# Kernel optimization log

Measured on AMD Instinct MI355X. Metric: run time of the kernel, lower is better.

## Reference

```python
import jax, jax.numpy as jnp
import numpy as np

B, C, H, W = 8, 256, 64, 64
DQK = 16  # int(sqrt(out_channels))


def setup_inputs() -> dict:
    key = jax.random.key(0)
    ks = jax.random.split(key, 8)
    s_in = 1.0 / np.sqrt(C)
    return {
        "x": jax.random.normal(ks[0], (B, C, H, W), dtype=jnp.float32),
        "Wf": jax.random.normal(ks[1], (DQK, C), dtype=jnp.float32) * s_in,
        "bf": jnp.zeros((DQK,), dtype=jnp.float32),
        "Wg": jax.random.normal(ks[2], (DQK, C), dtype=jnp.float32) * s_in,
        "bg": jnp.zeros((DQK,), dtype=jnp.float32),
        "Wh": jax.random.normal(ks[3], (C, C), dtype=jnp.float32) * s_in,
        "bh": jnp.zeros((C,), dtype=jnp.float32),
        # original inits attention_multiplier to 0.0; use small nonzero so output depends on attention path
        "gamma": jnp.float32(0.5),
    }


def reference(x, Wf, bf, Wg, bg, Wh, bh, gamma):
    b, c, h, w = x.shape
    hw = h * w
    # 1x1 convs == per-pixel channel projections
    f = (jnp.einsum('bchw,oc->bohw', x, Wf) + bf[None, :, None, None]).reshape(b, -1, hw)  # [B,DQK,HW]
    g = (jnp.einsum('bchw,oc->bohw', x, Wg) + bg[None, :, None, None]).reshape(b, -1, hw)  # [B,DQK,HW]
    hh = (jnp.einsum('bchw,oc->bohw', x, Wh) + bh[None, :, None, None]).reshape(b, -1, hw)  # [B,C,HW]
    # s[b,n,m] = sum_k g[b,k,n] * f[b,k,m]  -> [B,HW,HW]
    s = jnp.einsum('bkn,bkm->bnm', g, f)
    beta = jax.nn.softmax(s, axis=-1)
    # o = beta @ h^T, then transpose back to channel-first: [B,C,HW]
    o = jnp.einsum('bnm,bcm->bcn', beta, hh)
    return gamma * o.reshape(x.shape) + x
```

## Files before the change

### kernel.cpp

```cpp
#include <hip/hip_runtime.h>
#include <math.h>

#define BATCH 8
#define CH    256
#define HWN   4096
#define DQK   16

typedef __attribute__((ext_vector_type(8))) short short8;
typedef __attribute__((ext_vector_type(4))) float float4v;

__device__ __forceinline__ unsigned short f2bf(float f) {
    union { float f; unsigned int u; } v; v.f = f;
    unsigned int r = v.u + 0x7FFF + ((v.u >> 16) & 1);
    return (unsigned short)(r >> 16);
}
__device__ __forceinline__ unsigned int pack2bf(float lo, float hi) {
    union { float f; unsigned int u; } a, b; a.f = lo; b.f = hi;
    unsigned int ra = (a.u + 0x7FFF + ((a.u >> 16) & 1)) >> 16;
    unsigned int rb = (b.u + 0x7FFF + ((b.u >> 16) & 1)) & 0xFFFF0000u;
    return ra | rb;
}
__device__ __forceinline__ int perm_ft(int m) {
    return (m & ~28) | ((m & 24) >> 1) | ((m & 4) << 2);
}

__global__ __launch_bounds__(256) void wcast_kernel(
    const float* __restrict__ Wf, const float* __restrict__ bf_,
    const float* __restrict__ Wg, const float* __restrict__ bg,
    const float* __restrict__ Wh, const float* __restrict__ bh,
    unsigned short* __restrict__ Wbf, float* __restrict__ bcat)
{
    const int r = blockIdx.x;
    const int t = threadIdx.x;
    const float* src = (r < 16) ? (Wf + r*CH) : (r < 32) ? (Wg + (r-16)*CH) : (Wh + (r-32)*CH);
    Wbf[r*CH + t] = f2bf(src[t]);
    if (t == 0) bcat[r] = (r < 16) ? bf_[r] : (r < 32) ? bg[r-16] : bh[r-32];
}

__global__ __launch_bounds__(256) void xt_kernel(const float* __restrict__ x,
                                                 unsigned short* __restrict__ xt)
{
    const int t  = threadIdx.x;
    const int p0 = blockIdx.x * 64;
    const int c0 = blockIdx.y * 64;
    const int b  = blockIdx.z;
    __shared__ unsigned short tile[64][73];
    const int pc = t & 63;
    const int r0 = (t >> 6) * 16;
    #pragma unroll
    for (int j = 0; j < 16; j++) {
        int c = r0 + j;
        tile[pc][c] = f2bf(x[(size_t)(b*CH + c0 + c)*HWN + p0 + pc]);
    }
    __syncthreads();
    const int pr = t >> 2;
    const int cb = (t & 3) * 16;
    unsigned int outv[8];
    #pragma unroll
    for (int i = 0; i < 8; i++)
        outv[i] = (unsigned int)tile[pr][cb + 2*i] | ((unsigned int)tile[pr][cb + 2*i + 1] << 16);
    unsigned short* dst = &xt[(size_t)(b*HWN + p0 + pr)*CH + c0 + cb];
    *(uint4*)dst       = *(uint4*)&outv[0];
    *(uint4*)(dst + 8) = *(uint4*)&outv[4];
}

__global__ __launch_bounds__(256, 6) void proj_kernel(
    const unsigned short* __restrict__ xt, const unsigned short* __restrict__ Wbf,
    const float* __restrict__ bcat,
    unsigned short* __restrict__ ft, unsigned short* __restrict__ g,
    unsigned short* __restrict__ h3)
{
    const int t      = threadIdx.x;
    const int px0    = blockIdx.x * 64;
    const int b      = blockIdx.y;
    const int rtbase = blockIdx.z * 6;
    const int lane = t & 63, w = t >> 6, l15 = lane & 15, quad = lane >> 4;

    float4v acc[6];
    #pragma unroll
    for (int rt = 0; rt < 6; rt++) acc[rt] = (float4v){0.f,0.f,0.f,0.f};

    const unsigned short* xrow = &xt[((size_t)(b*HWN + px0 + w*16 + l15))*CH + quad*8];
    const unsigned short* wrow = &Wbf[(size_t)l15*CH + quad*8];

    #pragma unroll
    for (int ks = 0; ks < 8; ks++) {
        short8 afrag = *(const short8*)&xrow[ks*32];
        #pragma unroll
        for (int rt = 0; rt < 6; rt++) {
            short8 bfrag = *(const short8*)&wrow[(size_t)(rtbase + rt)*16*CH + ks*32];
            acc[rt] = __builtin_amdgcn_mfma_f32_16x16x32_bf16(afrag, bfrag, acc[rt], 0, 0, 0);
        }
    }

    const int pxl = px0 + w*16 + quad*4;
    const int mt  = (px0 >> 5) + (w >> 1);
    const int sub = ((w & 1)*2 + (quad >> 1))*128 + l15*8 + (quad & 1)*4;
    #pragma unroll
    for (int rt = 0; rt < 6; rt++) {
        const int R = rtbase + rt;
        if (R == 0) {
            float bv = bcat[l15];
            const int s0 = perm_ft(pxl);
            #pragma unroll
            for (int r = 0; r < 4; r++) {
                unsigned short* fp = &ft[((size_t)b*HWN + s0 + r)*32];
                fp[l15]      = f2bf(acc[rt][r] + bv);
                fp[16 + l15] = 0;
            }
        } else if (R == 1) {
            float bv = bcat[16 + l15];
            #pragma unroll
            for (int r = 0; r < 4; r++)
                g[(size_t)(b*DQK + l15)*HWN + pxl + r] = f2bf(acc[rt][r] + bv);
        } else {
            float bv = bcat[R*16 + l15];
            unsigned int u0 = pack2bf(acc[rt][0] + bv, acc[rt][1] + bv);
            unsigned int u1 = pack2bf(acc[rt][2] + bv, acc[rt][3] + bv);
            *(uint2*)&h3[(((size_t)((b*128 + mt)*16 + (R-2))) << 9) + sub] = make_uint2(u0, u1);
        }
    }
}

__global__ __launch_bounds__(512, 4) void attn_kernel(
    const unsigned short* __restrict__ ft, const unsigned short* __restrict__ g,
    const unsigned short* __restrict__ h3, const float* __restrict__ x,
    const float* __restrict__ gamma_p, float* __restrict__ out)
{
    const int t    = threadIdx.x;
    const int b    = blockIdx.x & 7;
    const int q0   = (blockIdx.x >> 3) * 64;
    const int lane = t & 63, w = t >> 6, l15 = lane & 15, quad = lane >> 4;
    const int qt_w = w >> 1, half = w & 1;

    __shared__ __align__(16) uint4 pB[2][2][4][64];
    __shared__ float l_l[4][16][2];

    union { short8 v; unsigned short u[8]; } gfrag;
    #pragma unroll
    for (int j = 0; j < 8; j++) {
        int k = quad*8 + j;
        gfrag.u[j] = (k < DQK) ? g[(size_t)(b*DQK + k)*HWN + q0 + qt_w*16 + l15] : (unsigned short)0;
    }

    const unsigned short* ftb = ft + (size_t)b*HWN*32;
    const unsigned short* h3b = h3 + ((size_t)b << 20);

    short8 fr[2][2], hr[2][2][2];
    float4v acc[2][4];
    #pragma unroll
    for (int i = 0; i < 2; i++)
        #pragma unroll
        for (int j = 0; j < 4; j++) acc[i][j] = (float4v){0.f,0.f,0.f,0.f};
    float l_acc = 0.f;

    #pragma unroll
    for (int j = 0; j < 2; j++)
        fr[0][j] = *(const short8*)&ftb[(size_t)((half*2 + j)*16 + l15)*32 + quad*8];
    #pragma unroll
    for (int grp = 0; grp < 2; grp++)
        #pragma unroll
        for (int ctl = 0; ctl < 2; ctl++)
            hr[0][grp][ctl] = *(const short8*)&h3b[(((size_t)(grp*16 + w*2 + ctl)) << 9) + lane*8];

    for (int i0 = 0; i0 < 64; i0 += 2) {
        #pragma unroll
        for (int u = 0; u < 2; u++) {
            const int i = i0 + u;
            float4v z = {0.f,0.f,0.f,0.f};
            float4v s[2];
            #pragma unroll
            for (int j = 0; j < 2; j++)
                s[j] = __builtin_amdgcn_mfma_f32_16x16x32_bf16(fr[u][j], gfrag.v, z, 0, 0, 0);
            unsigned int P[2][2];
            #pragma unroll
            for (int j = 0; j < 2; j++) {
                float e0 = __expf(s[j][0]), e1 = __expf(s[j][1]);
                float e2 = __expf(s[j][2]), e3 = __expf(s[j][3]);
                l_acc += (e0 + e1) + (e2 + e3);
                P[j][0] = pack2bf(e0, e1);
                P[j][1] = pack2bf(e2, e3);
            }
            pB[u][half][qt_w][lane] = make_uint4(P[0][0], P[0][1], P[1][0], P[1][1]);
            __syncthreads();
            const int ni = (i + 1) & 63;
            #pragma unroll
            for (int j = 0; j < 2; j++)
                fr[u^1][j] = *(const short8*)&ftb[(size_t)(ni*64 + (half*2 + j)*16 + l15)*32 + quad*8];
            #pragma unroll
            for (int grp = 0; grp < 2; grp++)
                #pragma unroll
                for (int ctl = 0; ctl < 2; ctl++)
                    hr[u^1][grp][ctl] = *(const short8*)&h3b[(((size_t)((ni*2 + grp)*16 + w*2 + ctl)) << 9) + lane*8];
            #pragma unroll
            for (int grp = 0; grp < 2; grp++) {
                #pragma unroll
                for (int qt = 0; qt < 4; qt++) {
                    union { uint4 uu; short8 v; } bq;
                    bq.uu = pB[u][grp][qt][lane];
                    #pragma unroll
                    for (int ctl = 0; ctl < 2; ctl++)
                        acc[ctl][qt] = __builtin_amdgcn_mfma_f32_16x16x32_bf16(hr[u][grp][ctl], bq.v, acc[ctl][qt], 0, 0, 0);
                }
            }
        }
    }

    l_acc += __shfl_xor(l_acc, 16, 64);
    l_acc += __shfl_xor(l_acc, 32, 64);
    if (quad == 0) l_l[qt_w][l15][half] = l_acc;
    __syncthreads();

    const float gamma = *gamma_p;
    float linv[4];
    #pragma unroll
    for (int qt = 0; qt < 4; qt++) linv[qt] = 1.f / (l_l[qt][l15][0] + l_l[qt][l15][1]);
    #pragma unroll
    for (int ctl = 0; ctl < 2; ctl++) {
        #pragma unroll
        for (int r = 0; r < 4; r++) {
            int c = w*32 + ctl*16 + quad*4 + r;
            size_t base = (size_t)(b*CH + c)*HWN + q0;
            #pragma unroll
            for (int qt = 0; qt < 4; qt++) {
                size_t o = base + qt*16 + l15;
                out[o] = gamma * acc[ctl][qt][r] * linv[qt] + x[o];
            }
        }
    }
}

extern "C" void kernel_launch(void* const* d_in, const int* in_sizes, int n_in,
                              void* d_out, int out_size, void* d_ws, size_t ws_size,
                              hipStream_t stream) {
    const float* x     = (const float*)d_in[0];
    const float* Wf    = (const float*)d_in[1];
    const float* bf_   = (const float*)d_in[2];
    const float* Wg    = (const float*)d_in[3];
    const float* bg    = (const float*)d_in[4];
    const float* Wh    = (const float*)d_in[5];
    const float* bh    = (const float*)d_in[6];
    const float* gamma = (const float*)d_in[7];
    float* out = (float*)d_out;

    unsigned short* xt   = (unsigned short*)d_ws;
    unsigned short* ftp  = xt  + (size_t)BATCH*HWN*CH;
    unsigned short* g    = ftp + (size_t)BATCH*HWN*32;
    unsigned short* h3   = g   + (size_t)BATCH*DQK*HWN;
    unsigned short* Wbf  = h3  + (size_t)BATCH*128*16*512;
    float*          bcat = (float*)(Wbf + 288*CH);

    wcast_kernel<<<dim3(288), 256, 0, stream>>>(Wf, bf_, Wg, bg, Wh, bh, Wbf, bcat);
    xt_kernel<<<dim3(HWN/64, CH/64, BATCH), 256, 0, stream>>>(x, xt);
    proj_kernel<<<dim3(HWN/64, BATCH, 3), 256, 0, stream>>>(xt, Wbf, bcat, ftp, g, h3);
    attn_kernel<<<dim3((HWN/64)*BATCH), 512, 0, stream>>>(ftp, g, h3, x, gamma, out);
}
```

Before: 223.9 us.

## Software-pipeline QK exp stage ahead of PV MFMAs and use hardware bf16 pack

Restructures the attention loop so the QK^T MFMA, exp and bf16 packing for the next key tile run before the PV MFMAs of the current tile, with the f tile prefetched two steps ahead. The aim is to overlap transcendental and conversion work with the matrix accumulation and to shorten the dependency chain around the barrier. It also replaces the manual round-to-nearest bf16 packing with the v_cvt_pk_bf16_f32 instruction and vectorizes the g stores in the projection kernel. The deeper prefetch adds register pressure, which matters at 512 threads with launch_bounds occupancy 4, and the inline asm ties the code to targets that provide this instruction.

```diff
diff --git a/kernel.cpp b/kernel.cpp
--- a/kernel.cpp
+++ b/kernel.cpp
@@ -14,11 +14,10 @@
     unsigned int r = v.u + 0x7FFF + ((v.u >> 16) & 1);
     return (unsigned short)(r >> 16);
 }
-__device__ __forceinline__ unsigned int pack2bf(float lo, float hi) {
-    union { float f; unsigned int u; } a, b; a.f = lo; b.f = hi;
-    unsigned int ra = (a.u + 0x7FFF + ((a.u >> 16) & 1)) >> 16;
-    unsigned int rb = (b.u + 0x7FFF + ((b.u >> 16) & 1)) & 0xFFFF0000u;
-    return ra | rb;
+__device__ __forceinline__ unsigned int cvtpk(float lo, float hi) {
+    unsigned int r;
+    asm("v_cvt_pk_bf16_f32 %0, %1, %2" : "=v"(r) : "v"(lo), "v"(hi));
+    return r;
 }
 __device__ __forceinline__ int perm_ft(int m) {
     return (m & ~28) | ((m & 24) >> 1) | ((m & 4) << 2);
@@ -102,21 +101,22 @@
         if (R == 0) {
             float bv = bcat[l15];
             const int s0 = perm_ft(pxl);
-            #pragma unroll
-            for (int r = 0; r < 4; r++) {
-                unsigned short* fp = &ft[((size_t)b*HWN + s0 + r)*32];
-                fp[l15]      = f2bf(acc[rt][r] + bv);
-                fp[16 + l15] = 0;
-            }
+            unsigned int p01 = cvtpk(acc[rt][0] + bv, acc[rt][1] + bv);
+            unsigned int p23 = cvtpk(acc[rt][2] + bv, acc[rt][3] + bv);
+            unsigned short* fp0 = &ft[((size_t)b*HWN + s0)*32];
+            fp0[l15]       = (unsigned short)p01;         fp0[16 + l15]  = 0;
+            fp0[32 + l15]  = (unsigned short)(p01 >> 16); fp0[48 + l15]  = 0;
+            fp0[64 + l15]  = (unsigned short)p23;         fp0[80 + l15]  = 0;
+            fp0[96 + l15]  = (unsigned short)(p23 >> 16); fp0[112 + l15] = 0;
         } else if (R == 1) {
             float bv = bcat[16 + l15];
-            #pragma unroll
-            for (int r = 0; r < 4; r++)
-                g[(size_t)(b*DQK + l15)*HWN + pxl + r] = f2bf(acc[rt][r] + bv);
+            unsigned int a01 = cvtpk(acc[rt][0] + bv, acc[rt][1] + bv);
+            unsigned int a23 = cvtpk(acc[rt][2] + bv, acc[rt][3] + bv);
+            *(uint2*)&g[(size_t)(b*DQK + l15)*HWN + pxl] = make_uint2(a01, a23);
         } else {
             float bv = bcat[R*16 + l15];
-            unsigned int u0 = pack2bf(acc[rt][0] + bv, acc[rt][1] + bv);
-            unsigned int u1 = pack2bf(acc[rt][2] + bv, acc[rt][3] + bv);
+            unsigned int u0 = cvtpk(acc[rt][0] + bv, acc[rt][1] + bv);
+            unsigned int u1 = cvtpk(acc[rt][2] + bv, acc[rt][3] + bv);
             *(uint2*)&h3[(((size_t)((b*128 + mt)*16 + (R-2))) << 9) + sub] = make_uint2(u0, u1);
         }
     }
@@ -153,58 +153,71 @@
         #pragma unroll
         for (int j = 0; j < 4; j++) acc[i][j] = (float4v){0.f,0.f,0.f,0.f};
     float l_acc = 0.f;
+    uint4 P;
 
     #pragma unroll
     for (int j = 0; j < 2; j++)
         fr[0][j] = *(const short8*)&ftb[(size_t)((half*2 + j)*16 + l15)*32 + quad*8];
+    {
+        float4v z = {0.f,0.f,0.f,0.f};
+        float4v s0v = __builtin_amdgcn_mfma_f32_16x16x32_bf16(fr[0][0], gfrag.v, z, 0, 0, 0);
+        float4v s1v = __builtin_amdgcn_mfma_f32_16x16x32_bf16(fr[0][1], gfrag.v, z, 0, 0, 0);
+        float e0 = __expf(s0v[0]), e1 = __expf(s0v[1]), e2 = __expf(s0v[2]), e3 = __expf(s0v[3]);
+        float e4 = __expf(s1v[0]), e5 = __expf(s1v[1]), e6 = __expf(s1v[2]), e7 = __expf(s1v[3]);
+        l_acc += (e0 + e1) + (e2 + e3) + (e4 + e5) + (e6 + e7);
+        P = make_uint4(cvtpk(e0, e1), cvtpk(e2, e3), cvtpk(e4, e5), cvtpk(e6, e7));
+    }
+    #pragma unroll
+    for (int j = 0; j < 2; j++)
+        fr[1][j] = *(const short8*)&ftb[(size_t)(64 + (half*2 + j)*16 + l15)*32 + quad*8];
     #pragma unroll
     for (int grp = 0; grp < 2; grp++)
         #pragma unroll
         for (int ctl = 0; ctl < 2; ctl++)
             hr[0][grp][ctl] = *(const short8*)&h3b[(((size_t)(grp*16 + w*2 + ctl)) << 9) + lane*8];
 
-    for (int i0 = 0; i0 < 64; i0 += 2) {
-        #pragma unroll
-        for (int u = 0; u < 2; u++) {
-            const int i = i0 + u;
-            float4v z = {0.f,0.f,0.f,0.f};
-            float4v s[2];
-            #pragma unroll
-            for (int j = 0; j < 2; j++)
-                s[j] = __builtin_amdgcn_mfma_f32_16x16x32_bf16(fr[u][j], gfrag.v, z, 0, 0, 0);
-            unsigned int P[2][2];
-            #pragma unroll
-            for (int j = 0; j < 2; j++) {
-                float e0 = __expf(s[j][0]), e1 = __expf(s[j][1]);
-                float e2 = __expf(s[j][2]), e3 = __expf(s[j][3]);
-                l_acc += (e0 + e1) + (e2 + e3);
-                P[j][0] = pack2bf(e0, e1);
-                P[j][1] = pack2bf(e2, e3);
-            }
-            pB[u][half][qt_w][lane] = make_uint4(P[0][0], P[0][1], P[1][0], P[1][1]);
-            __syncthreads();
-            const int ni = (i + 1) & 63;
-            #pragma unroll
-            for (int j = 0; j < 2; j++)
-                fr[u^1][j] = *(const short8*)&ftb[(size_t)(ni*64 + (half*2 + j)*16 + l15)*32 + quad*8];
-            #pragma unroll
-            for (int grp = 0; grp < 2; grp++)
-                #pragma unroll
-                for (int ctl = 0; ctl < 2; ctl++)
-                    hr[u^1][grp][ctl] = *(const short8*)&h3b[(((size_t)((ni*2 + grp)*16 + w*2 + ctl)) << 9) + lane*8];
-            #pragma unroll
-            for (int grp = 0; grp < 2; grp++) {
-                #pragma unroll
-                for (int qt = 0; qt < 4; qt++) {
-                    union { uint4 uu; short8 v; } bq;
-                    bq.uu = pB[u][grp][qt][lane];
-                    #pragma unroll
-                    for (int ctl = 0; ctl < 2; ctl++)
-                        acc[ctl][qt] = __builtin_amdgcn_mfma_f32_16x16x32_bf16(hr[u][grp][ctl], bq.v, acc[ctl][qt], 0, 0, 0);
-                }
-            }
-        }
-    }
+#define ATTN_STEP(u, i, DO_NEXT) do {                                          \
+    pB[u][half][qt_w][lane] = P;                                               \
+    __syncthreads();                                                           \
+    if (DO_NEXT) {                                                             \
+      const int nf = ((i) + 2) & 63;                                           \
+      _Pragma("unroll")                                                        \
+      for (int j = 0; j < 2; j++)                                              \
+        fr[u][j] = *(const short8*)&ftb[(size_t)(nf*64 + (half*2 + j)*16 + l15)*32 + quad*8]; \
+      const int nh = ((i) + 1) & 63;                                           \
+      _Pragma("unroll")                                                        \
+      for (int grp = 0; grp < 2; grp++)                                        \
+        _Pragma("unroll")                                                      \
+        for (int ctl = 0; ctl < 2; ctl++)                                      \
+          hr[(u)^1][grp][ctl] = *(const short8*)&h3b[(((size_t)((nh*2 + grp)*16 + w*2 + ctl)) << 9) + lane*8]; \
+      float4v z = {0.f,0.f,0.f,0.f};                                           \
+      float4v s0v = __builtin_amdgcn_mfma_f32_16x16x32_bf16(fr[(u)^1][0], gfrag.v, z, 0, 0, 0); \
+      float4v s1v = __builtin_amdgcn_mfma_f32_16x16x32_bf16(fr[(u)^1][1], gfrag.v, z, 0, 0, 0); \
+      float e0 = __expf(s0v[0]), e1 = __expf(s0v[1]), e2 = __expf(s0v[2]), e3 = __expf(s0v[3]); \
+      float e4 = __expf(s1v[0]), e5 = __expf(s1v[1]), e6 = __expf(s1v[2]), e7 = __expf(s1v[3]); \
+      l_acc += (e0 + e1) + (e2 + e3) + (e4 + e5) + (e6 + e7);                  \
+      P = make_uint4(cvtpk(e0, e1), cvtpk(e2, e3), cvtpk(e4, e5), cvtpk(e6, e7)); \
+    }                                                                          \
+    _Pragma("unroll")                                                          \
+    for (int grp = 0; grp < 2; grp++) {                                        \
+      _Pragma("unroll")                                                        \
+      for (int qt = 0; qt < 4; qt++) {                                         \
+        union { uint4 uu; short8 v; } bq;                                      \
+        bq.uu = pB[u][grp][qt][lane];                                          \
+        _Pragma("unroll")                                                      \
+        for (int ctl = 0; ctl < 2; ctl++)                                      \
+          acc[ctl][qt] = __builtin_amdgcn_mfma_f32_16x16x32_bf16(hr[u][grp][ctl], bq.v, acc[ctl][qt], 0, 0, 0); \
+      }                                                                        \
+    }                                                                          \
+  } while (0)
+
+    for (int i0 = 0; i0 < 62; i0 += 2) {
+        ATTN_STEP(0, i0, 1);
+        ATTN_STEP(1, i0 + 1, 1);
+    }
+    ATTN_STEP(0, 62, 1);
+    ATTN_STEP(1, 63, 0);
+#undef ATTN_STEP
 
     l_acc += __shfl_xor(l_acc, 16, 64);
     l_acc += __shfl_xor(l_acc, 32, 64);
```

New measurement: 217.3 us. 1.03x faster.
